# Optimization experiments

Measured on AMD Instinct MI355X. Metric: run time of the kernel, lower is better.

Reference implementation:

```python
import jax, jax.numpy as jnp
import numpy as np
from functools import partial

BATCH, SEQ = 2, 2048
D_MODEL, D_INNER, D_XB = 2048, 4096, 1024
HEADDIM, D_STATE = 64, 64
NHEADS = D_INNER // HEADDIM      # 64
NKV = D_XB // HEADDIM            # 16
REP = NHEADS // NKV              # 4
INTER = 8192
EPS = 1e-5
D_IN_PROJ = D_INNER + D_XB + D_XB + D_INNER + NHEADS  # z, x, B, C, dt


def setup_inputs() -> dict:
    key = jax.random.key(0)
    ks = jax.random.split(key, 8)
    g = lambda k, shape, s: (jax.random.normal(k, shape, jnp.float32) * s)
    return {
        "hidden_states": g(ks[0], (BATCH, SEQ, D_MODEL), 1.0),
        "ln_w": jnp.ones((D_MODEL,), jnp.float32),
        "ln_b": jnp.zeros((D_MODEL,), jnp.float32),
        "in_proj_w": g(ks[1], (D_IN_PROJ, D_MODEL), 0.02),
        "dt_bias": jax.random.uniform(ks[2], (NHEADS,), jnp.float32, -4.0, 0.0),
        "A_log": jnp.log(jnp.arange(1, NHEADS + 1, dtype=jnp.float32)),
        "Dp": jnp.ones((NHEADS,), jnp.float32),
        "norm_w": jnp.ones((D_INNER,), jnp.float32),
        "out_proj_w": g(ks[3], (D_MODEL, D_INNER), 0.02),
        "fc1_w": g(ks[4], (INTER, D_MODEL), 0.02),
        "fc1_b": jnp.zeros((INTER,), jnp.float32),
        "fc2_w": g(ks[5], (D_MODEL, INTER), 0.02),
        "fc2_b": jnp.zeros((D_MODEL,), jnp.float32),
    }


def _layernorm(x, w, b):
    mu = x.mean(-1, keepdims=True)
    var = ((x - mu) ** 2).mean(-1, keepdims=True)
    return (x - mu) * jax.lax.rsqrt(var + EPS) * w + b


def _ssd_scan(xh, dt, A, Bh, Ch):
    # xh: (b,l,h,p)  dt: (b,l,h)  A: (h,)  Bh,Ch: (b,l,h,n)
    dA = jnp.exp(dt * A)  # (b,l,h) discrete decay
    to_l = lambda t: jnp.moveaxis(t, 1, 0)  # time-major for scan

    def step(state, inp):
        dA_t, dt_t, x_t, B_t, C_t = inp
        state = state * dA_t[:, :, None, None] + jnp.einsum(
            "bh,bhp,bhn->bhpn", dt_t, x_t, B_t)
        y = jnp.einsum("bhpn,bhn->bhp", state, C_t)
        return state, y

    state0 = jnp.zeros((xh.shape[0], NHEADS, HEADDIM, D_STATE), xh.dtype)
    _, ys = jax.lax.scan(step, state0, (to_l(dA), to_l(dt), to_l(xh), to_l(Bh), to_l(Ch)))
    return jnp.moveaxis(ys, 0, 1)  # (b,l,h,p)


def reference(hidden_states, ln_w, ln_b, in_proj_w, dt_bias, A_log, Dp,
              norm_w, out_proj_w, fc1_w, fc1_b, fc2_w, fc2_b):
    residual = hidden_states
    h = _layernorm(hidden_states, ln_w, ln_b)

    # ---- Mamba2 branch ----
    zxbcdt = h @ in_proj_w.T  # (b,l,D_IN_PROJ)
    z, x, Bm, Cm, dt = jnp.split(
        zxbcdt, np.cumsum([D_INNER, D_XB, D_XB, D_INNER]).tolist(), axis=-1)
    b, l = h.shape[0], h.shape[1]
    dt = jax.nn.softplus(dt + dt_bias)               # (b,l,nheads)
    A = -jnp.exp(A_log)                              # (nheads,)
    # GQA-style repeat of x (values) and B (keys) from NKV to NHEADS groups
    xh = jnp.repeat(x.reshape(b, l, NKV, HEADDIM), REP, axis=2)   # (b,l,h,p)
    Bh = jnp.repeat(Bm.reshape(b, l, NKV, D_STATE), REP, axis=2)  # (b,l,h,n)
    Ch = Cm.reshape(b, l, NHEADS, D_STATE)                        # (b,l,h,n)

    y = _ssd_scan(xh, dt, A, Bh, Ch) + Dp[None, None, :, None] * xh
    yf = y.reshape(b, l, D_INNER)
    # gated RMSNorm (norm_before_gate=False): gate first, then rmsnorm
    yf = yf * jax.nn.silu(z)
    yf = yf * jax.lax.rsqrt((yf * yf).mean(-1, keepdims=True) + EPS) * norm_w
    mamba_out = yf @ out_proj_w.T

    # ---- Phi MLP branch (parallel, shares the layernormed input) ----
    mlp = jax.nn.gelu(h @ fc1_w.T + fc1_b, approximate=True) @ fc2_w.T + fc2_b

    # resid_dropout is identity in eval mode
    return mamba_out + mlp + residual
```

## Files before the change

### kernel.cpp

```cpp
#include <hip/hip_runtime.h>
#include <hip/hip_bf16.h>

#define BATCH 2
#define SEQ   2048
#define DMODEL 2048
#define DINNER 4096
#define DXB   1024
#define NHEADS 64
#define NKV   16
#define HEADDIM 64
#define DSTATE 64
#define INTER 8192
#define DINPROJ 10304
#define ROWS  (BATCH*SEQ)
#define NC    32
#define EPSV  1e-5f

typedef short short8 __attribute__((ext_vector_type(8)));
typedef float f32x4 __attribute__((ext_vector_type(4)));

typedef const __attribute__((address_space(1))) unsigned int cg_u32;
typedef __attribute__((address_space(3))) unsigned int ls_u32;

static __device__ __forceinline__ void gll16(const void* g, void* l) {
    __builtin_amdgcn_global_load_lds((cg_u32*)g, (ls_u32*)l, 16, 0, 0);
}

static __device__ __forceinline__ unsigned short f2bf(float f) {
    unsigned int u = __float_as_uint(f);
    unsigned int r = (u + 0x7fffu + ((u >> 16) & 1u)) >> 16;
    return (unsigned short)r;
}
static __device__ __forceinline__ float bf2f(unsigned short h) {
    return __uint_as_float(((unsigned int)h) << 16);
}

__global__ __launch_bounds__(256) void convk(const float* __restrict__ in,
                                             unsigned short* __restrict__ out, int n4) {
    int stride = gridDim.x * blockDim.x;
    for (int i = blockIdx.x * blockDim.x + threadIdx.x; i < n4; i += stride) {
        float4 v = ((const float4*)in)[i];
        ushort4 o;
        o.x = f2bf(v.x); o.y = f2bf(v.y); o.z = f2bf(v.z); o.w = f2bf(v.w);
        ((ushort4*)out)[i] = o;
    }
}

__global__ __launch_bounds__(256) void ln_kernel(const float* __restrict__ x,
                                                 const float* __restrict__ w,
                                                 const float* __restrict__ b,
                                                 unsigned short* __restrict__ hout) {
    int row = blockIdx.x;
    int t = threadIdx.x;
    const float* xr = x + (size_t)row * DMODEL;
    float v[8];
    float4 v0 = *(const float4*)&xr[t * 8];
    float4 v1 = *(const float4*)&xr[t * 8 + 4];
    v[0]=v0.x; v[1]=v0.y; v[2]=v0.z; v[3]=v0.w; v[4]=v1.x; v[5]=v1.y; v[6]=v1.z; v[7]=v1.w;
    float s = 0.f, s2 = 0.f;
    #pragma unroll
    for (int i = 0; i < 8; ++i) { s += v[i]; s2 += v[i]*v[i]; }
    #pragma unroll
    for (int off = 1; off < 64; off <<= 1) { s += __shfl_xor(s, off); s2 += __shfl_xor(s2, off); }
    __shared__ float sa[4], sb[4];
    int lane = t & 63, wv = t >> 6;
    if (lane == 0) { sa[wv] = s; sb[wv] = s2; }
    __syncthreads();
    s = sa[0]+sa[1]+sa[2]+sa[3];
    s2 = sb[0]+sb[1]+sb[2]+sb[3];
    float mu = s / DMODEL;
    float var = s2 / DMODEL - mu * mu;
    float sc = rsqrtf(var + EPSV);
    unsigned short* ho = hout + (size_t)row * DMODEL + t * 8;
    #pragma unroll
    for (int i = 0; i < 8; ++i) {
        int d = t * 8 + i;
        ho[i] = f2bf((v[i] - mu) * sc * w[d] + b[d]);
    }
}

#define SLOTSZ 49152
template <int EPI>
__global__ __launch_bounds__(512, 2) void gemm_p(
    const unsigned short* __restrict__ A, const unsigned short* __restrict__ B,
    int M, int N, int K, int nby,
    float* __restrict__ outF, unsigned short* __restrict__ outH,
    const float* __restrict__ bias, const float* __restrict__ add1,
    const float* __restrict__ add2) {
    __shared__ __align__(16) char smem[3 * SLOTSZ];
    int t = threadIdx.x, lane = t & 63, w = t >> 6;
    int nwg = gridDim.x, cpx = nwg >> 3;
    int logical = (blockIdx.x & 7) * cpx + (blockIdx.x >> 3);
    int by = logical % nby, bx = logical / nby;
    int brow = by * 128, bcol = bx * 256;
    int wr = w >> 2, wc = w & 3;
    int wrb = wr * 64, wcb = wc * 64;

    int lr8 = lane >> 3;
    int lch = ((lane & 7) ^ lr8) << 3;
    const unsigned short* pa[2];
    #pragma unroll
    for (int j = 0; j < 2; ++j)
        pa[j] = A + (size_t)(brow + w * 16 + j * 8 + lr8) * K + lch;
    const unsigned short* pb[4];
    #pragma unroll
    for (int j = 0; j < 4; ++j) {
        int r = bcol + w * 32 + j * 8 + lr8;
        if (r > N - 1) r = N - 1;
        pb[j] = B + (size_t)r * K + lch;
    }
    auto stageA = [&](int slot, int j) {
        gll16(pa[j], smem + slot * SLOTSZ + (w * 16 + j * 8) * 128);
        pa[j] += 64;
    };
    auto stageB = [&](int slot, int j) {
        gll16(pb[j], smem + slot * SLOTSZ + 16384 + (w * 32 + j * 8) * 128);
        pb[j] += 64;
    };

    int arow = lane & 15;
    int swz0 = (((lane >> 4) ^ (lane & 7)) << 4);

    f32x4 acc[4][4] = {};
    const int NT = K >> 6;
    #pragma unroll
    for (int j = 0; j < 2; ++j) stageA(0, j);
    #pragma unroll
    for (int j = 0; j < 4; ++j) stageB(0, j);
    #pragma unroll
    for (int j = 0; j < 2; ++j) stageA(1, j);
    #pragma unroll
    for (int j = 0; j < 4; ++j) stageB(1, j);
    asm volatile("s_waitcnt vmcnt(6)" ::: "memory");
    __builtin_amdgcn_s_barrier();
    asm volatile("" ::: "memory");

    int slot = 0, slot2 = 2;
    for (int kt = 0; kt < NT; ++kt) {
        const char* Ab = smem + slot * SLOTSZ;
        const char* Bb = Ab + 16384;
        bool st = (kt + 2 < NT);
        short8 af[4], bfv[4];
        #pragma unroll
        for (int f = 0; f < 4; ++f)
            af[f] = *(const short8*)(Ab + (wrb + f * 16 + arow) * 128 + swz0);
        #pragma unroll
        for (int n = 0; n < 4; ++n)
            bfv[n] = *(const short8*)(Bb + (wcb + n * 16 + arow) * 128 + swz0);
        if (st) { stageA(slot2, 0); stageA(slot2, 1); stageB(slot2, 0); }
        __builtin_amdgcn_s_barrier();
        asm volatile("s_waitcnt lgkmcnt(0)" ::: "memory");
        __builtin_amdgcn_sched_barrier(0);
        __builtin_amdgcn_s_setprio(1);
        #pragma unroll
        for (int f = 0; f < 4; ++f)
            #pragma unroll
            for (int n = 0; n < 4; ++n)
                acc[f][n] = __builtin_amdgcn_mfma_f32_16x16x32_bf16(af[f], bfv[n], acc[f][n], 0, 0, 0);
        __builtin_amdgcn_s_setprio(0);
        __builtin_amdgcn_s_barrier();
        #pragma unroll
        for (int f = 0; f < 4; ++f)
            af[f] = *(const short8*)(Ab + (wrb + f * 16 + arow) * 128 + (swz0 ^ 64));
        #pragma unroll
        for (int n = 0; n < 4; ++n)
            bfv[n] = *(const short8*)(Bb + (wcb + n * 16 + arow) * 128 + (swz0 ^ 64));
        if (st) { stageB(slot2, 1); stageB(slot2, 2); stageB(slot2, 3); }
        __builtin_amdgcn_s_barrier();
        asm volatile("s_waitcnt lgkmcnt(0)" ::: "memory");
        __builtin_amdgcn_sched_barrier(0);
        __builtin_amdgcn_s_setprio(1);
        #pragma unroll
        for (int f = 0; f < 4; ++f)
            #pragma unroll
            for (int n = 0; n < 4; ++n)
                acc[f][n] = __builtin_amdgcn_mfma_f32_16x16x32_bf16(af[f], bfv[n], acc[f][n], 0, 0, 0);
        __builtin_amdgcn_s_setprio(0);
        if (kt + 2 < NT)      asm volatile("s_waitcnt vmcnt(6)" ::: "memory");
        else if (kt + 1 < NT) asm volatile("s_waitcnt vmcnt(0)" ::: "memory");
        __builtin_amdgcn_s_barrier();
        asm volatile("" ::: "memory");
        slot  = (slot  == 2) ? 0 : slot + 1;
        slot2 = (slot2 == 2) ? 0 : slot2 + 1;
    }

    int rlane = (lane >> 4) << 2, clane = lane & 15;
    #pragma unroll
    for (int f = 0; f < 4; ++f) {
        #pragma unroll
        for (int n = 0; n < 4; ++n) {
            int col = bcol + wcb + n * 16 + clane;
            if (col < N) {
                #pragma unroll
                for (int j = 0; j < 4; ++j) {
                    int row = brow + wrb + f * 16 + rlane + j;
                    size_t idx = (size_t)row * N + col;
                    float v = acc[f][n][j];
                    if constexpr (EPI == 0) {
                        outF[idx] = v;
                    } else if constexpr (EPI == 1) {
                        v += bias[col];
                        float g = 0.5f * v * (1.f + tanhf(0.7978845608f * (v + 0.044715f * v * v * v)));
                        outH[idx] = f2bf(g);
                    } else if constexpr (EPI == 2) {
                        outF[idx] = v + bias[col] + add1[idx] + add2[idx];
                    } else {
                        outH[idx] = f2bf(v);
                    }
                }
            }
        }
    }
}

static __device__ __forceinline__ void mm64(const unsigned short* Al, const unsigned short* Bl,
                                            f32x4* acc, int w, int lane) {
    int lr = lane & 15, kg = (lane >> 4) << 3;
    #pragma unroll
    for (int ks = 0; ks < 2; ++ks) {
        short8 a = *(const short8*)&Al[(w * 16 + lr) * 64 + ks * 32 + kg];
        #pragma unroll
        for (int fn = 0; fn < 4; ++fn) {
            short8 bb = *(const short8*)&Bl[(fn * 16 + lr) * 64 + ks * 32 + kg];
            acc[fn] = __builtin_amdgcn_mfma_f32_16x16x32_bf16(a, bb, acc[fn], 0, 0, 0);
        }
    }
}

__global__ __launch_bounds__(256) void chunk_front(const unsigned short* __restrict__ zx,
                                                   const float* __restrict__ dt_bias,
                                                   const float* __restrict__ A_log,
                                                   float* __restrict__ pcum,
                                                   unsigned short* __restrict__ ybuf,
                                                   unsigned short* __restrict__ Sbuf) {
    __shared__ __align__(16) unsigned short Cs[64*64], Bsr[64*64], Btr[64*64],
                                            Xtr[64*64], Xw[64*64], Wsm[64*64];
    __shared__ float dts[64], clg[64];
    int t = threadIdx.x, lane = t & 63, w = t >> 6;
    int bid = blockIdx.x;
    int c = bid & 31, h = (bid >> 5) & 63, b = bid >> 11, g = h >> 2;
    int row0 = (b << 11) + (c << 6);

    if (t < 64) {
        float raw = bf2f(zx[(size_t)(row0 + t) * DINPROJ + 10240 + h]) + dt_bias[h];
        float dt = raw > 20.f ? raw : log1pf(expf(raw));
        dts[t] = dt;
        float v = dt * (-expf(A_log[h]));
        #pragma unroll
        for (int off = 1; off < 64; off <<= 1) {
            float o = __shfl_up(v, off);
            if (lane >= off) v += o;
        }
        clg[t] = v;
        pcum[(size_t)(row0 + t) * 64 + h] = expf(v);
    }
    ushort4 xr[4];
    #pragma unroll
    for (int i = 0; i < 4; ++i) {
        int q = i * 256 + t, s = q >> 4, d4 = (q & 15) << 2;
        const unsigned short* rp = zx + (size_t)(row0 + s) * DINPROJ;
        ushort4 cv = *(const ushort4*)&rp[6144 + h * 64 + d4];
        *(ushort4*)&Cs[s * 64 + d4] = cv;
        ushort4 bv = *(const ushort4*)&rp[5120 + g * 64 + d4];
        *(ushort4*)&Bsr[s * 64 + d4] = bv;
        Btr[(d4 + 0) * 64 + s] = bv.x; Btr[(d4 + 1) * 64 + s] = bv.y;
        Btr[(d4 + 2) * 64 + s] = bv.z; Btr[(d4 + 3) * 64 + s] = bv.w;
        ushort4 xv = *(const ushort4*)&rp[4096 + g * 64 + d4];
        Xtr[(d4 + 0) * 64 + s] = xv.x; Xtr[(d4 + 1) * 64 + s] = xv.y;
        Xtr[(d4 + 2) * 64 + s] = xv.z; Xtr[(d4 + 3) * 64 + s] = xv.w;
        xr[i] = xv;
    }
    __syncthreads();
    float cl63 = clg[63];
    #pragma unroll
    for (int i = 0; i < 4; ++i) {
        int q = i * 256 + t, s = q >> 4, d4 = (q & 15) << 2;
        float ws = dts[s] * expf(cl63 - clg[s]);
        Xw[(d4 + 0) * 64 + s] = f2bf(bf2f(xr[i].x) * ws);
        Xw[(d4 + 1) * 64 + s] = f2bf(bf2f(xr[i].y) * ws);
        Xw[(d4 + 2) * 64 + s] = f2bf(bf2f(xr[i].z) * ws);
        Xw[(d4 + 3) * 64 + s] = f2bf(bf2f(xr[i].w) * ws);
    }
    __syncthreads();
    f32x4 accG[4] = {};
    mm64(Cs, Bsr, accG, w, lane);
    int rl = (lane >> 4) << 2, cl = lane & 15;
    #pragma unroll
    for (int fn = 0; fn < 4; ++fn) {
        #pragma unroll
        for (int j = 0; j < 4; ++j) {
            int tr = w * 16 + rl + j, rc = fn * 16 + cl;
            float val = 0.f;
            if (rc <= tr) val = accG[fn][j] * expf(clg[tr] - clg[rc]) * dts[rc];
            Wsm[tr * 64 + rc] = f2bf(val);
        }
    }
    __syncthreads();
    f32x4 accY[4] = {};
    mm64(Wsm, Xtr, accY, w, lane);
    f32x4 accS[4] = {};
    mm64(Xw, Btr, accS, w, lane);
    size_t cb = (size_t)((((b << 6) + h) << 5) + c) * 4096;
    #pragma unroll
    for (int fn = 0; fn < 4; ++fn) {
        #pragma unroll
        for (int j = 0; j < 4; ++j) {
            int tr = w * 16 + rl + j, pc = fn * 16 + cl;
            ybuf[(size_t)(row0 + tr) * DINNER + h * 64 + pc] = f2bf(accY[fn][j]);
            Sbuf[cb + tr * 64 + pc] = f2bf(accS[fn][j]);
        }
    }
}

__global__ __launch_bounds__(256) void chunk_state(unsigned short* __restrict__ SH,
                                                   const float* __restrict__ pcum) {
    int b = blockIdx.x >> 6, h = blockIdx.x & 63, t = threadIdx.x;
    float H[16];
    #pragma unroll
    for (int j = 0; j < 16; ++j) H[j] = 0.f;
    for (int c = 0; c < NC; ++c) {
        size_t base = (size_t)((((b << 6) + h) << 5) + c) * 4096;
        float Tc = pcum[(size_t)((b << 11) + (c << 6) + 63) * 64 + h];
        #pragma unroll
        for (int j = 0; j < 16; ++j) {
            int e = j * 256 + t;
            unsigned short sv = SH[base + e];
            SH[base + e] = f2bf(H[j]);
            H[j] = H[j] * Tc + bf2f(sv);
        }
    }
}

__global__ __launch_bounds__(256) void chunk_back(const unsigned short* __restrict__ zx,
                                                  const unsigned short* __restrict__ SH,
                                                  const float* __restrict__ pcum,
                                                  const float* __restrict__ Dp,
                                                  unsigned short* __restrict__ ybuf) {
    __shared__ __align__(16) unsigned short Cs[64*64], Hs[64*64];
    __shared__ float ps[64];
    int t = threadIdx.x, lane = t & 63, w = t >> 6;
    int bid = blockIdx.x;
    int c = bid & 31, h = (bid >> 5) & 63, b = bid >> 11, g = h >> 2;
    int row0 = (b << 11) + (c << 6);
    size_t cb = (size_t)((((b << 6) + h) << 5) + c) * 4096;
    #pragma unroll
    for (int i = 0; i < 4; ++i) {
        int q = i * 256 + t, s = q >> 4, d4 = (q & 15) << 2;
        *(ushort4*)&Cs[s * 64 + d4] =
            *(const ushort4*)&zx[(size_t)(row0 + s) * DINPROJ + 6144 + h * 64 + d4];
        *(ushort4*)&Hs[s * 64 + d4] = *(const ushort4*)&SH[cb + s * 64 + d4];
    }
    if (t < 64) ps[t] = pcum[(size_t)(row0 + t) * 64 + h];
    __syncthreads();
    f32x4 acc[4] = {};
    mm64(Cs, Hs, acc, w, lane);
    float Dph = Dp[h];
    int rl = (lane >> 4) << 2, cl = lane & 15;
    #pragma unroll
    for (int fn = 0; fn < 4; ++fn) {
        #pragma unroll
        for (int j = 0; j < 4; ++j) {
            int tr = w * 16 + rl + j, pc = fn * 16 + cl;
            size_t yi = (size_t)(row0 + tr) * DINNER + h * 64 + pc;
            float xv = bf2f(zx[(size_t)(row0 + tr) * DINPROJ + 4096 + g * 64 + pc]);
            ybuf[yi] = f2bf(bf2f(ybuf[yi]) + acc[fn][j] * ps[tr] + Dph * xv);
        }
    }
}

__global__ __launch_bounds__(256) void gate_kernel(const unsigned short* __restrict__ y,
                                                   const unsigned short* __restrict__ zx,
                                                   const float* __restrict__ norm_w,
                                                   unsigned short* __restrict__ yf) {
    int row = blockIdx.x;
    int t = threadIdx.x;
    float v[16];
    float s2 = 0.f;
    #pragma unroll
    for (int i = 0; i < 16; ++i) {
        int d = i * 256 + t;
        float yv = bf2f(y[(size_t)row * DINNER + d]);
        float zv = bf2f(zx[(size_t)row * DINPROJ + d]);
        float gt = zv / (1.f + expf(-zv));
        v[i] = yv * gt;
        s2 += v[i] * v[i];
    }
    #pragma unroll
    for (int off = 1; off < 64; off <<= 1) s2 += __shfl_xor(s2, off);
    __shared__ float sb[4];
    int lane = t & 63, wv = t >> 6;
    if (lane == 0) sb[wv] = s2;
    __syncthreads();
    s2 = sb[0] + sb[1] + sb[2] + sb[3];
    float sc = rsqrtf(s2 / DINNER + EPSV);
    #pragma unroll
    for (int i = 0; i < 16; ++i) {
        int d = i * 256 + t;
        yf[(size_t)row * DINNER + d] = f2bf(v[i] * sc * norm_w[d]);
    }
}

extern "C" void kernel_launch(void* const* d_in, const int* in_sizes, int n_in,
                              void* d_out, int out_size, void* d_ws, size_t ws_size,
                              hipStream_t stream) {
    const float* hid   = (const float*)d_in[0];
    const float* ln_w  = (const float*)d_in[1];
    const float* ln_b  = (const float*)d_in[2];
    const float* w_inp = (const float*)d_in[3];
    const float* dtb   = (const float*)d_in[4];
    const float* A_log = (const float*)d_in[5];
    const float* Dp    = (const float*)d_in[6];
    const float* nw    = (const float*)d_in[7];
    const float* w_out = (const float*)d_in[8];
    const float* w_fc1 = (const float*)d_in[9];
    const float* fc1_b = (const float*)d_in[10];
    const float* w_fc2 = (const float*)d_in[11];
    const float* fc2_b = (const float*)d_in[12];

    char* ws = (char*)d_ws;
    size_t off = 0;
    auto alloc = [&](size_t bytes) { size_t o = off; off += (bytes + 255) & ~(size_t)255; return o; };
    size_t o_h    = alloc((size_t)ROWS * DMODEL * 2);
    size_t o_w    = alloc((size_t)DINPROJ * DMODEL * 2);
    size_t o_zx   = alloc((size_t)ROWS * DINPROJ * 2);
    size_t o_pc   = alloc((size_t)ROWS * NHEADS * 4);
    size_t o_y    = alloc((size_t)ROWS * DINNER * 2);
    size_t o_yf   = alloc((size_t)ROWS * DINNER * 2);
    size_t o_S    = alloc((size_t)BATCH * NHEADS * NC * HEADDIM * DSTATE * 2);

    unsigned short* h_bf  = (unsigned short*)(ws + o_h);
    unsigned short* wbuf  = (unsigned short*)(ws + o_w);
    unsigned short* zx    = (unsigned short*)(ws + o_zx);
    float* pcum           = (float*)(ws + o_pc);
    unsigned short* ybuf  = (unsigned short*)(ws + o_y);
    unsigned short* yf    = (unsigned short*)(ws + o_yf);
    unsigned short* Sbuf  = (unsigned short*)(ws + o_S);
    unsigned short* gelu  = (unsigned short*)(ws + o_zx);
    float* mamba          = (float*)(ws + o_y);
    float* outF           = (float*)d_out;

    ln_kernel<<<ROWS, 256, 0, stream>>>(hid, ln_w, ln_b, h_bf);
    convk<<<2048, 256, 0, stream>>>(w_inp, wbuf, (DINPROJ * DMODEL) / 4);
    gemm_p<3><<<41 * 32, 512, 0, stream>>>(
        h_bf, wbuf, ROWS, DINPROJ, DMODEL, 32, nullptr, zx, nullptr, nullptr, nullptr);
    chunk_front<<<BATCH * NHEADS * NC, 256, 0, stream>>>(zx, dtb, A_log, pcum, ybuf, Sbuf);
    chunk_state<<<BATCH * NHEADS, 256, 0, stream>>>(Sbuf, pcum);
    chunk_back<<<BATCH * NHEADS * NC, 256, 0, stream>>>(zx, Sbuf, pcum, Dp, ybuf);
    gate_kernel<<<ROWS, 256, 0, stream>>>(ybuf, zx, nw, yf);
    convk<<<2048, 256, 0, stream>>>(w_out, wbuf, (DMODEL * DINNER) / 4);
    gemm_p<0><<<8 * 32, 512, 0, stream>>>(
        yf, wbuf, ROWS, DMODEL, DINNER, 32, mamba, nullptr, nullptr, nullptr, nullptr);
    convk<<<2048, 256, 0, stream>>>(w_fc1, wbuf, (INTER * DMODEL) / 4);
    gemm_p<1><<<32 * 32, 512, 0, stream>>>(
        h_bf, wbuf, ROWS, INTER, DMODEL, 32, nullptr, gelu, fc1_b, nullptr, nullptr);
    convk<<<2048, 256, 0, stream>>>(w_fc2, wbuf, (DMODEL * INTER) / 4);
    gemm_p<2><<<8 * 32, 512, 0, stream>>>(
        gelu, wbuf, ROWS, DMODEL, INTER, 32, outF, nullptr, fc2_b, mamba, hid);
}
```

Measured before the change: 838.8 us.

## Enlarge GEMM tile to 256x256 with double-buffered LDS pipeline

Changes the GEMM block tile from 128x256 to 256x256, so each wave computes 128x64 outputs with 8x4 accumulators. The three-slot staggered staging scheme is replaced by a simple two-buffer pipeline: wait for all loads, barrier, prefetch the next K tile, then do two k-substeps. The aim is more reuse per LDS load and fewer workgroups. The cost is a wait on all outstanding loads each iteration, more registers at 2 waves/SIMD, 128KB of LDS, and half as many blocks, which can leave CUs idle on the smaller GEMMs.

Result: slower. 881.7 us (+5.1%).

```diff
diff --git a/kernel.cpp b/kernel.cpp
--- a/kernel.cpp
+++ b/kernel.cpp
@@ -79,7 +79,7 @@
     }
 }
 
-#define SLOTSZ 49152
+#define BUFSZ 65536
 template <int EPI>
 __global__ __launch_bounds__(512, 2) void gemm_p(
     const unsigned short* __restrict__ A, const unsigned short* __restrict__ B,
@@ -87,21 +87,21 @@
     float* __restrict__ outF, unsigned short* __restrict__ outH,
     const float* __restrict__ bias, const float* __restrict__ add1,
     const float* __restrict__ add2) {
-    __shared__ __align__(16) char smem[3 * SLOTSZ];
+    __shared__ __align__(16) char smem[2 * BUFSZ];
     int t = threadIdx.x, lane = t & 63, w = t >> 6;
     int nwg = gridDim.x, cpx = nwg >> 3;
     int logical = (blockIdx.x & 7) * cpx + (blockIdx.x >> 3);
     int by = logical % nby, bx = logical / nby;
-    int brow = by * 128, bcol = bx * 256;
+    int brow = by * 256, bcol = bx * 256;
     int wr = w >> 2, wc = w & 3;
-    int wrb = wr * 64, wcb = wc * 64;
+    int wrb = wr * 128, wcb = wc * 64;
 
     int lr8 = lane >> 3;
     int lch = ((lane & 7) ^ lr8) << 3;
-    const unsigned short* pa[2];
-    #pragma unroll
-    for (int j = 0; j < 2; ++j)
-        pa[j] = A + (size_t)(brow + w * 16 + j * 8 + lr8) * K + lch;
+    const unsigned short* pa[4];
+    #pragma unroll
+    for (int j = 0; j < 4; ++j)
+        pa[j] = A + (size_t)(brow + w * 32 + j * 8 + lr8) * K + lch;
     const unsigned short* pb[4];
     #pragma unroll
     for (int j = 0; j < 4; ++j) {
@@ -109,84 +109,55 @@
         if (r > N - 1) r = N - 1;
         pb[j] = B + (size_t)r * K + lch;
     }
-    auto stageA = [&](int slot, int j) {
-        gll16(pa[j], smem + slot * SLOTSZ + (w * 16 + j * 8) * 128);
-        pa[j] += 64;
+    auto stage = [&](int buf) {
+        #pragma unroll
+        for (int j = 0; j < 4; ++j) {
+            gll16(pa[j], smem + buf * BUFSZ + (w * 32 + j * 8) * 128);
+            pa[j] += 64;
+        }
+        #pragma unroll
+        for (int j = 0; j < 4; ++j) {
+            gll16(pb[j], smem + buf * BUFSZ + 32768 + (w * 32 + j * 8) * 128);
+            pb[j] += 64;
+        }
     };
-    auto stageB = [&](int slot, int j) {
-        gll16(pb[j], smem + slot * SLOTSZ + 16384 + (w * 32 + j * 8) * 128);
-        pb[j] += 64;
-    };
 
     int arow = lane & 15;
-    int swz0 = (((lane >> 4) ^ (lane & 7)) << 4);
-
-    f32x4 acc[4][4] = {};
+    int kq = lane >> 4;
+
+    f32x4 acc[8][4] = {};
     const int NT = K >> 6;
-    #pragma unroll
-    for (int j = 0; j < 2; ++j) stageA(0, j);
-    #pragma unroll
-    for (int j = 0; j < 4; ++j) stageB(0, j);
-    #pragma unroll
-    for (int j = 0; j < 2; ++j) stageA(1, j);
-    #pragma unroll
-    for (int j = 0; j < 4; ++j) stageB(1, j);
-    asm volatile("s_waitcnt vmcnt(6)" ::: "memory");
-    __builtin_amdgcn_s_barrier();
-    asm volatile("" ::: "memory");
-
-    int slot = 0, slot2 = 2;
+    stage(0);
     for (int kt = 0; kt < NT; ++kt) {
-        const char* Ab = smem + slot * SLOTSZ;
-        const char* Bb = Ab + 16384;
-        bool st = (kt + 2 < NT);
-        short8 af[4], bfv[4];
-        #pragma unroll
-        for (int f = 0; f < 4; ++f)
-            af[f] = *(const short8*)(Ab + (wrb + f * 16 + arow) * 128 + swz0);
-        #pragma unroll
-        for (int n = 0; n < 4; ++n)
-            bfv[n] = *(const short8*)(Bb + (wcb + n * 16 + arow) * 128 + swz0);
-        if (st) { stageA(slot2, 0); stageA(slot2, 1); stageB(slot2, 0); }
+        asm volatile("s_waitcnt vmcnt(0)" ::: "memory");
         __builtin_amdgcn_s_barrier();
-        asm volatile("s_waitcnt lgkmcnt(0)" ::: "memory");
-        __builtin_amdgcn_sched_barrier(0);
-        __builtin_amdgcn_s_setprio(1);
-        #pragma unroll
-        for (int f = 0; f < 4; ++f)
+        asm volatile("" ::: "memory");
+        const char* Ab = smem + (kt & 1) * BUFSZ;
+        const char* Bb = Ab + 32768;
+        if (kt + 1 < NT) stage((kt + 1) & 1);
+        #pragma unroll
+        for (int ks = 0; ks < 2; ++ks) {
+            int sw = (((ks << 2) | kq) ^ (arow & 7)) << 4;
+            short8 af[8], bfv[4];
+            #pragma unroll
+            for (int f = 0; f < 8; ++f)
+                af[f] = *(const short8*)(Ab + (wrb + f * 16 + arow) * 128 + sw);
             #pragma unroll
             for (int n = 0; n < 4; ++n)
-                acc[f][n] = __builtin_amdgcn_mfma_f32_16x16x32_bf16(af[f], bfv[n], acc[f][n], 0, 0, 0);
-        __builtin_amdgcn_s_setprio(0);
-        __builtin_amdgcn_s_barrier();
-        #pragma unroll
-        for (int f = 0; f < 4; ++f)
-            af[f] = *(const short8*)(Ab + (wrb + f * 16 + arow) * 128 + (swz0 ^ 64));
-        #pragma unroll
-        for (int n = 0; n < 4; ++n)
-            bfv[n] = *(const short8*)(Bb + (wcb + n * 16 + arow) * 128 + (swz0 ^ 64));
-        if (st) { stageB(slot2, 1); stageB(slot2, 2); stageB(slot2, 3); }
-        __builtin_amdgcn_s_barrier();
-        asm volatile("s_waitcnt lgkmcnt(0)" ::: "memory");
-        __builtin_amdgcn_sched_barrier(0);
-        __builtin_amdgcn_s_setprio(1);
-        #pragma unroll
-        for (int f = 0; f < 4; ++f)
+                bfv[n] = *(const short8*)(Bb + (wcb + n * 16 + arow) * 128 + sw);
+            __builtin_amdgcn_s_setprio(1);
             #pragma unroll
-            for (int n = 0; n < 4; ++n)
-                acc[f][n] = __builtin_amdgcn_mfma_f32_16x16x32_bf16(af[f], bfv[n], acc[f][n], 0, 0, 0);
-        __builtin_amdgcn_s_setprio(0);
-        if (kt + 2 < NT)      asm volatile("s_waitcnt vmcnt(6)" ::: "memory");
-        else if (kt + 1 < NT) asm volatile("s_waitcnt vmcnt(0)" ::: "memory");
-        __builtin_amdgcn_s_barrier();
-        asm volatile("" ::: "memory");
-        slot  = (slot  == 2) ? 0 : slot + 1;
-        slot2 = (slot2 == 2) ? 0 : slot2 + 1;
+            for (int f = 0; f < 8; ++f)
+                #pragma unroll
+                for (int n = 0; n < 4; ++n)
+                    acc[f][n] = __builtin_amdgcn_mfma_f32_16x16x32_bf16(af[f], bfv[n], acc[f][n], 0, 0, 0);
+            __builtin_amdgcn_s_setprio(0);
+        }
     }
 
     int rlane = (lane >> 4) << 2, clane = lane & 15;
     #pragma unroll
-    for (int f = 0; f < 4; ++f) {
+    for (int f = 0; f < 8; ++f) {
         #pragma unroll
         for (int n = 0; n < 4; ++n) {
             int col = bcol + wcb + n * 16 + clane;
@@ -441,19 +412,19 @@
 
     ln_kernel<<<ROWS, 256, 0, stream>>>(hid, ln_w, ln_b, h_bf);
     convk<<<2048, 256, 0, stream>>>(w_inp, wbuf, (DINPROJ * DMODEL) / 4);
-    gemm_p<3><<<41 * 32, 512, 0, stream>>>(
-        h_bf, wbuf, ROWS, DINPROJ, DMODEL, 32, nullptr, zx, nullptr, nullptr, nullptr);
+    gemm_p<3><<<41 * 16, 512, 0, stream>>>(
+        h_bf, wbuf, ROWS, DINPROJ, DMODEL, 16, nullptr, zx, nullptr, nullptr, nullptr);
     chunk_front<<<BATCH * NHEADS * NC, 256, 0, stream>>>(zx, dtb, A_log, pcum, ybuf, Sbuf);
     chunk_state<<<BATCH * NHEADS, 256, 0, stream>>>(Sbuf, pcum);
     chunk_back<<<BATCH * NHEADS * NC, 256, 0, stream>>>(zx, Sbuf, pcum, Dp, ybuf);
     gate_kernel<<<ROWS, 256, 0, stream>>>(ybuf, zx, nw, yf);
     convk<<<2048, 256, 0, stream>>>(w_out, wbuf, (DMODEL * DINNER) / 4);
-    gemm_p<0><<<8 * 32, 512, 0, stream>>>(
-        yf, wbuf, ROWS, DMODEL, DINNER, 32, mamba, nullptr, nullptr, nullptr, nullptr);
+    gemm_p<0><<<8 * 16, 512, 0, stream>>>(
+        yf, wbuf, ROWS, DMODEL, DINNER, 16, mamba, nullptr, nullptr, nullptr, nullptr);
     convk<<<2048, 256, 0, stream>>>(w_fc1, wbuf, (INTER * DMODEL) / 4);
-    gemm_p<1><<<32 * 32, 512, 0, stream>>>(
-        h_bf, wbuf, ROWS, INTER, DMODEL, 32, nullptr, gelu, fc1_b, nullptr, nullptr);
+    gemm_p<1><<<32 * 16, 512, 0, stream>>>(
+        h_bf, wbuf, ROWS, INTER, DMODEL, 16, nullptr, gelu, fc1_b, nullptr, nullptr);
     convk<<<2048, 256, 0, stream>>>(w_fc2, wbuf, (DMODEL * INTER) / 4);
-    gemm_p<2><<<8 * 32, 512, 0, stream>>>(
-        gelu, wbuf, ROWS, DMODEL, INTER, 32, outF, nullptr, fc2_b, mamba, hid);
-}
+    gemm_p<2><<<8 * 16, 512, 0, stream>>>(
+        gelu, wbuf, ROWS, DMODEL, INTER, 16, outF, nullptr, fc2_b, mamba, hid);
+}
```
